# Kernel tuning notes

Hardware: AMD Instinct MI355X
Metric: run time of the kernel (lower is better)

Reference implementation:

```python
import jax, jax.numpy as jnp
import numpy as np

WIDTH = 32
DEPTH = 4
N_NODES = 50000
N_EDGES = 1600000


def setup_inputs() -> dict:
    key = jax.random.key(0)
    ks = jax.random.split(key, 10)
    N, E, W = N_NODES, N_EDGES, WIDTH
    s = 0.1
    x = jax.random.normal(ks[0], (N, 3), dtype=jnp.float32)
    edge_index = jax.random.randint(ks[1], (2, E), 0, N, dtype=jnp.int64)
    edge_attr = jax.random.uniform(ks[2], (E, 3), dtype=jnp.float32)
    # fc1: Linear(3, W); fc2: Linear(W, 1)
    fc1_w = jax.random.normal(ks[3], (W, 3), dtype=jnp.float32) * s
    fc1_b = jnp.zeros((W,), jnp.float32)
    fc2_w = jax.random.normal(ks[4], (1, W), dtype=jnp.float32) * s
    fc2_b = jnp.zeros((1,), jnp.float32)
    # 3 structurally distinct NNConv layers (reused DEPTH times), stacked on axis 0.
    # Edge-kernel MLP: Linear(3, W//4) -> ReLU -> Linear(W//4, W)
    kw1 = jax.random.normal(ks[5], (3, W // 4, 3), dtype=jnp.float32) * s
    kb1 = jnp.zeros((3, W // 4), jnp.float32)
    kw2 = jax.random.normal(ks[6], (3, W, W // 4), dtype=jnp.float32) * s
    kb2 = jnp.zeros((3, W), jnp.float32)
    # NNConv root weight [in, out] and bias
    root = jax.random.normal(ks[7], (3, W, W), dtype=jnp.float32) * s
    cbias = jnp.zeros((3, W), jnp.float32)
    return {"x": x, "edge_index": edge_index, "edge_attr": edge_attr,
            "fc1_w": fc1_w, "fc1_b": fc1_b, "fc2_w": fc2_w, "fc2_b": fc2_b,
            "kw1": kw1, "kb1": kb1, "kw2": kw2, "kb2": kb2,
            "root": root, "cbias": cbias}


def reference(x, edge_index, edge_attr, fc1_w, fc1_b, fc2_w, fc2_b,
              kw1, kb1, kw2, kb2, root, cbias):
    N = x.shape[0]
    src, dst = edge_index[0], edge_index[1]
    # in-degree counts for scatter-mean (clamped to 1 like PyG)
    counts = jax.ops.segment_sum(jnp.ones(dst.shape[0], x.dtype), dst, num_segments=N)
    inv_counts = 1.0 / jnp.maximum(counts, 1.0)

    h = x @ fc1_w.T + fc1_b  # [N, W]
    for _ in range(DEPTH):
        for c in range(3):
            # diagonal NNConv: edge MLP -> per-edge weight vector [E, W]
            w = jax.nn.relu(edge_attr @ kw1[c].T + kb1[c]) @ kw2[c].T + kb2[c]
            msg = h[src] * w                      # gather + elementwise per-edge product
            agg = jax.ops.segment_sum(msg, dst, num_segments=N) * inv_counts[:, None]
            h = jax.nn.relu(agg + h @ root[c] + cbias[c])
    return h @ fc2_w.T + fc2_b  # [N, 1]
```

## Files before the change

kernel.cpp:

```cpp
#include <hip/hip_runtime.h>

#define WN 32
#define HID 8
#define DEPTH 4
#define GPB 16

typedef float fvec4 __attribute__((ext_vector_type(4)));

__global__ void zero_kernel(int* __restrict__ cnt, int* __restrict__ cursor, int n) {
    int i = blockIdx.x * blockDim.x + threadIdx.x;
    if (i < n) { cnt[i] = 0; cursor[i] = 0; }
}

__global__ void count_kernel(const int* __restrict__ eidx, int* __restrict__ cnt, int e_cnt) {
    int e = blockIdx.x * blockDim.x + threadIdx.x;
    if (e >= e_cnt) return;
    atomicAdd(&cnt[eidx[e_cnt + e]], 1);
}

__global__ void scan_kernel(const int* __restrict__ cnt, int* __restrict__ row_ptr,
                            float* __restrict__ inv, int n) {
    __shared__ int s_wave[16];
    int t = threadIdx.x;
    int lane = t & 63;
    int wv = t >> 6;
    int offset = 0;
    for (int base = 0; base < n; base += 1024) {
        int i = base + t;
        int v = (i < n) ? cnt[i] : 0;
        int x = v;
#pragma unroll
        for (int d = 1; d < 64; d <<= 1) {
            int y = __shfl_up(x, d, 64);
            if (lane >= d) x += y;
        }
        if (lane == 63) s_wave[wv] = x;
        __syncthreads();
        if (wv == 0 && lane < 16) {
            int y = s_wave[lane];
#pragma unroll
            for (int d = 1; d < 16; d <<= 1) {
                int z = __shfl_up(y, d, 64);
                if (lane >= d) y += z;
            }
            s_wave[lane] = y;
        }
        __syncthreads();
        int waveoff = (wv > 0) ? s_wave[wv - 1] : 0;
        int total = s_wave[15];
        int incl = x + waveoff + offset;
        if (i < n) {
            row_ptr[i + 1] = incl;
            inv[i] = 1.0f / (float)(v > 1 ? v : 1);
        }
        offset += total;
        __syncthreads();
    }
    if (t == 0) row_ptr[0] = 0;
}

__global__ void scatter_kernel(const int* __restrict__ eidx, const float* __restrict__ ea,
                               const int* __restrict__ row_ptr, int* __restrict__ cursor,
                               fvec4* __restrict__ rec, int e_cnt) {
    int e = blockIdx.x * blockDim.x + threadIdx.x;
    if (e >= e_cnt) return;
    int src = eidx[e];
    int dst = eidx[e_cnt + e];
    int pos = row_ptr[dst] + atomicAdd(&cursor[dst], 1);
    fvec4 r;
    r.x = __int_as_float(src);
    r.y = ea[3 * e];
    r.z = ea[3 * e + 1];
    r.w = ea[3 * e + 2];
    rec[pos] = r;
}

__global__ void h0_kernel(const float* __restrict__ x, const float* __restrict__ fc1_w,
                          const float* __restrict__ fc1_b, float* __restrict__ h, int n) {
    __shared__ float s_w[WN * 3];
    __shared__ float s_b[WN];
    int t = threadIdx.x;
    if (t < WN * 3) s_w[t] = fc1_w[t];
    if (t < WN) s_b[t] = fc1_b[t];
    __syncthreads();
    int i = blockIdx.x * blockDim.x + t;
    if (i >= n) return;
    float x0 = x[3 * i], x1 = x[3 * i + 1], x2 = x[3 * i + 2];
#pragma unroll
    for (int j = 0; j < WN; j++) {
        h[(size_t)i * WN + j] = s_b[j] + s_w[j * 3] * x0 + s_w[j * 3 + 1] * x1 + s_w[j * 3 + 2] * x2;
    }
}

__global__ void gather2_kernel(const int* __restrict__ row_ptr, const fvec4* __restrict__ rec,
                               const float* __restrict__ h_in, float* __restrict__ h_out,
                               const float* __restrict__ inv,
                               const float* __restrict__ kw1, const float* __restrict__ kb1,
                               const float* __restrict__ kw2, const float* __restrict__ kb2,
                               const float* __restrict__ root, const float* __restrict__ cbias,
                               int n) {
    __shared__ float s_root[WN * 34];
    __shared__ float s_h[GPB * 34];
    __shared__ int   s_src[GPB][33];
    __shared__ fvec4 s_hid_u[GPB][33];
    __shared__ fvec4 s_hid_v[GPB][33];
    __shared__ int   s_maxdeg;

    int t = threadIdx.x;
    if (t == 0) s_maxdeg = 0;
    for (int i = t; i < WN * WN; i += 256) s_root[(i >> 5) * 34 + (i & 31)] = root[i];

    int grp = t >> 4;
    int tc  = t & 15;
    int node = blockIdx.x * GPB + grp;
    bool valid = node < n;

    const fvec4* kwp = (const fvec4*)(kw2 + tc * 16);
    fvec4 wa0 = kwp[0], wa1 = kwp[1];
    fvec4 wb0 = kwp[2], wb1 = kwp[3];
    float2 b2 = *(const float2*)(kb2 + 2 * tc);
    float2 cb = *(const float2*)(cbias + 2 * tc);

    int e0 = 0, e1 = 0;
    float2 hself = {0.0f, 0.0f};
    if (valid) {
        e0 = row_ptr[node];
        e1 = row_ptr[node + 1];
        hself = *(const float2*)(h_in + (size_t)node * WN + 2 * tc);
    }
    *(float2*)&s_h[grp * 34 + 2 * tc] = hself;
    int deg = e1 - e0;
    __syncthreads();
    if (valid && tc == 0 && deg > 0) atomicMax(&s_maxdeg, deg);
    __syncthreads();
    int nchunk = (s_maxdeg + 31) >> 5;

    float acc0 = 0.0f, acc1 = 0.0f;
    for (int cs = 0; cs < nchunk; cs++) {
        int ebase = e0 + (cs << 5);
#pragma unroll
        for (int s = 0; s < 2; s++) {
            int li = tc + (s << 4);
            int e = ebase + li;
            if (e < e1) {
                fvec4 r = rec[e];
                s_src[grp][li] = __float_as_int(r.x);
                float hv[HID];
#pragma unroll
                for (int j = 0; j < HID; j++) {
                    float u = kb1[j] + kw1[3 * j] * r.y + kw1[3 * j + 1] * r.z + kw1[3 * j + 2] * r.w;
                    hv[j] = u > 0.0f ? u : 0.0f;
                }
                fvec4 lo, hi;
                lo.x = hv[0]; lo.y = hv[1]; lo.z = hv[2]; lo.w = hv[3];
                hi.x = hv[4]; hi.y = hv[5]; hi.z = hv[6]; hi.w = hv[7];
                s_hid_u[grp][li] = lo;
                s_hid_v[grp][li] = hi;
            }
        }
        __syncthreads();
        int rem = e1 - ebase;
        int cnt = rem < 32 ? rem : 32;
#pragma unroll 4
        for (int i = 0; i < cnt; i++) {
            int src = s_src[grp][i];
            fvec4 u = s_hid_u[grp][i];
            fvec4 v = s_hid_v[grp][i];
            float w0 = b2.x + wa0.x * u.x + wa0.y * u.y + wa0.z * u.z + wa0.w * u.w
                            + wa1.x * v.x + wa1.y * v.y + wa1.z * v.z + wa1.w * v.w;
            float w1 = b2.y + wb0.x * u.x + wb0.y * u.y + wb0.z * u.z + wb0.w * u.w
                            + wb1.x * v.x + wb1.y * v.y + wb1.z * v.z + wb1.w * v.w;
            float2 hh = *(const float2*)(h_in + (size_t)src * WN + 2 * tc);
            acc0 += hh.x * w0;
            acc1 += hh.y * w1;
        }
        __syncthreads();
    }
    if (!valid) return;

    float invn = inv[node];
    float r0 = acc0 * invn + cb.x;
    float r1 = acc1 * invn + cb.y;
#pragma unroll
    for (int k = 0; k < WN; k++) {
        float hk = s_h[grp * 34 + k];
        float2 rt = *(const float2*)&s_root[k * 34 + 2 * tc];
        r0 += hk * rt.x;
        r1 += hk * rt.y;
    }
    float2 o;
    o.x = r0 > 0.0f ? r0 : 0.0f;
    o.y = r1 > 0.0f ? r1 : 0.0f;
    *(float2*)(h_out + (size_t)node * WN + 2 * tc) = o;
}

__global__ void out_kernel(const float* __restrict__ h, const float* __restrict__ fc2_w,
                           const float* __restrict__ fc2_b, float* __restrict__ out, int n) {
    __shared__ float s_w[WN];
    __shared__ float s_b;
    int t = threadIdx.x;
    if (t < WN) s_w[t] = fc2_w[t];
    if (t == 0) s_b = fc2_b[0];
    __syncthreads();
    int i = blockIdx.x * blockDim.x + t;
    if (i >= n) return;
    float acc = s_b;
#pragma unroll
    for (int k = 0; k < WN; k++) acc += h[(size_t)i * WN + k] * s_w[k];
    out[i] = acc;
}

extern "C" void kernel_launch(void* const* d_in, const int* in_sizes, int n_in,
                              void* d_out, int out_size, void* d_ws, size_t ws_size,
                              hipStream_t stream) {
    const float* x      = (const float*)d_in[0];
    const int*   eidx   = (const int*)d_in[1];
    const float* ea     = (const float*)d_in[2];
    const float* fc1_w  = (const float*)d_in[3];
    const float* fc1_b  = (const float*)d_in[4];
    const float* fc2_w  = (const float*)d_in[5];
    const float* fc2_b  = (const float*)d_in[6];
    const float* kw1    = (const float*)d_in[7];
    const float* kb1    = (const float*)d_in[8];
    const float* kw2    = (const float*)d_in[9];
    const float* kb2    = (const float*)d_in[10];
    const float* root   = (const float*)d_in[11];
    const float* cbias  = (const float*)d_in[12];
    float* out = (float*)d_out;

    const int n = in_sizes[0] / 3;
    const int e_cnt = in_sizes[2] / 3;

    auto pad4 = [](size_t v) { return (v + 3) & ~(size_t)3; };
    float* ws = (float*)d_ws;
    size_t off = 0;
    float* hA       = ws + off; off += pad4((size_t)n * WN);
    float* hB       = ws + off; off += pad4((size_t)n * WN);
    float* inv      = ws + off; off += pad4(n);
    int*   cnt      = (int*)(ws + off); off += pad4(n);
    int*   cursor   = (int*)(ws + off); off += pad4(n);
    int*   row_ptr  = (int*)(ws + off); off += pad4(n + 1);
    fvec4* rec      = (fvec4*)(ws + off); off += (size_t)4 * e_cnt;

    const int B = 256;
    int grid_n  = (n + B - 1) / B;
    int grid_e  = (e_cnt + B - 1) / B;
    int grid_g  = (n + GPB - 1) / GPB;

    zero_kernel<<<grid_n, B, 0, stream>>>(cnt, cursor, n);
    count_kernel<<<grid_e, B, 0, stream>>>(eidx, cnt, e_cnt);
    scan_kernel<<<1, 1024, 0, stream>>>(cnt, row_ptr, inv, n);
    scatter_kernel<<<grid_e, B, 0, stream>>>(eidx, ea, row_ptr, cursor, rec, e_cnt);
    h0_kernel<<<grid_n, B, 0, stream>>>(x, fc1_w, fc1_b, hA, n);

    float* hin = hA;
    float* hout = hB;
    for (int d = 0; d < DEPTH; d++) {
        for (int c = 0; c < 3; c++) {
            gather2_kernel<<<grid_g, B, 0, stream>>>(
                row_ptr, rec, hin, hout, inv,
                kw1 + (size_t)c * HID * 3, kb1 + (size_t)c * HID,
                kw2 + (size_t)c * WN * HID, kb2 + (size_t)c * WN,
                root + (size_t)c * WN * WN, cbias + (size_t)c * WN, n);
            float* tmp = hin; hin = hout; hout = tmp;
        }
    }
    out_kernel<<<grid_n, B, 0, stream>>>(hin, fc2_w, fc2_b, out, n);
}
```

Before: 764.0 us.

## Sort nodes by in-degree for load-balanced gather and drop shared root staging

Adds a degree histogram, a bin scan and an ordering pass so each gather block processes 16 nodes with similar in-degree, which cuts wasted iterations up to the block's max degree. It also drops the per-block shared-memory copy of the root matrix and reads root from global/L1 inside the final matvec. The cost is three extra preprocessing kernels, scattered node accesses through the order indirection, and possibly more global loads in the root product.

```diff
diff --git a/kernel.cpp b/kernel.cpp
--- a/kernel.cpp
+++ b/kernel.cpp
@@ -4,12 +4,15 @@
 #define HID 8
 #define DEPTH 4
 #define GPB 16
+#define NBIN 1024
 
 typedef float fvec4 __attribute__((ext_vector_type(4)));
 
-__global__ void zero_kernel(int* __restrict__ cnt, int* __restrict__ cursor, int n) {
+__global__ void zero_kernel(int* __restrict__ cnt, int* __restrict__ cursor,
+                            int* __restrict__ bins, int* __restrict__ bin_cursor, int n) {
     int i = blockIdx.x * blockDim.x + threadIdx.x;
     if (i < n) { cnt[i] = 0; cursor[i] = 0; }
+    if (i < NBIN) { bins[i] = 0; bin_cursor[i] = 0; }
 }
 
 __global__ void count_kernel(const int* __restrict__ eidx, int* __restrict__ cnt, int e_cnt) {
@@ -19,7 +22,7 @@
 }
 
 __global__ void scan_kernel(const int* __restrict__ cnt, int* __restrict__ row_ptr,
-                            float* __restrict__ inv, int n) {
+                            float* __restrict__ inv, int* __restrict__ bins, int n) {
     __shared__ int s_wave[16];
     int t = threadIdx.x;
     int lane = t & 63;
@@ -52,11 +55,51 @@
         if (i < n) {
             row_ptr[i + 1] = incl;
             inv[i] = 1.0f / (float)(v > 1 ? v : 1);
+            int d = v < (NBIN - 1) ? v : (NBIN - 1);
+            atomicAdd(&bins[d], 1);
         }
         offset += total;
         __syncthreads();
     }
     if (t == 0) row_ptr[0] = 0;
+}
+
+__global__ void bin_scan_kernel(const int* __restrict__ bins, int* __restrict__ bin_base) {
+    __shared__ int s_wave[16];
+    int t = threadIdx.x;
+    int lane = t & 63;
+    int wv = t >> 6;
+    int v = bins[t];
+    int x = v;
+#pragma unroll
+    for (int d = 1; d < 64; d <<= 1) {
+        int y = __shfl_up(x, d, 64);
+        if (lane >= d) x += y;
+    }
+    if (lane == 63) s_wave[wv] = x;
+    __syncthreads();
+    if (wv == 0 && lane < 16) {
+        int y = s_wave[lane];
+#pragma unroll
+        for (int d = 1; d < 16; d <<= 1) {
+            int z = __shfl_up(y, d, 64);
+            if (lane >= d) y += z;
+        }
+        s_wave[lane] = y;
+    }
+    __syncthreads();
+    int waveoff = (wv > 0) ? s_wave[wv - 1] : 0;
+    bin_base[t] = x + waveoff - v;
+}
+
+__global__ void order_kernel(const int* __restrict__ cnt, const int* __restrict__ bin_base,
+                             int* __restrict__ bin_cursor, int* __restrict__ order, int n) {
+    int i = blockIdx.x * blockDim.x + threadIdx.x;
+    if (i >= n) return;
+    int v = cnt[i];
+    int d = v < (NBIN - 1) ? v : (NBIN - 1);
+    int pos = bin_base[d] + atomicAdd(&bin_cursor[d], 1);
+    order[pos] = i;
 }
 
 __global__ void scatter_kernel(const int* __restrict__ eidx, const float* __restrict__ ea,
@@ -93,13 +136,13 @@
 }
 
 __global__ void gather2_kernel(const int* __restrict__ row_ptr, const fvec4* __restrict__ rec,
+                               const int* __restrict__ order,
                                const float* __restrict__ h_in, float* __restrict__ h_out,
                                const float* __restrict__ inv,
                                const float* __restrict__ kw1, const float* __restrict__ kb1,
                                const float* __restrict__ kw2, const float* __restrict__ kb2,
                                const float* __restrict__ root, const float* __restrict__ cbias,
                                int n) {
-    __shared__ float s_root[WN * 34];
     __shared__ float s_h[GPB * 34];
     __shared__ int   s_src[GPB][33];
     __shared__ fvec4 s_hid_u[GPB][33];
@@ -108,12 +151,12 @@
 
     int t = threadIdx.x;
     if (t == 0) s_maxdeg = 0;
-    for (int i = t; i < WN * WN; i += 256) s_root[(i >> 5) * 34 + (i & 31)] = root[i];
 
     int grp = t >> 4;
     int tc  = t & 15;
-    int node = blockIdx.x * GPB + grp;
-    bool valid = node < n;
+    int idx = blockIdx.x * GPB + grp;
+    bool valid = idx < n;
+    int node = valid ? order[idx] : 0;
 
     const fvec4* kwp = (const fvec4*)(kw2 + tc * 16);
     fvec4 wa0 = kwp[0], wa1 = kwp[1];
@@ -184,7 +227,7 @@
 #pragma unroll
     for (int k = 0; k < WN; k++) {
         float hk = s_h[grp * 34 + k];
-        float2 rt = *(const float2*)&s_root[k * 34 + 2 * tc];
+        float2 rt = *(const float2*)(root + k * WN + 2 * tc);
         r0 += hk * rt.x;
         r1 += hk * rt.y;
     }
@@ -234,22 +277,28 @@
     auto pad4 = [](size_t v) { return (v + 3) & ~(size_t)3; };
     float* ws = (float*)d_ws;
     size_t off = 0;
-    float* hA       = ws + off; off += pad4((size_t)n * WN);
-    float* hB       = ws + off; off += pad4((size_t)n * WN);
-    float* inv      = ws + off; off += pad4(n);
-    int*   cnt      = (int*)(ws + off); off += pad4(n);
-    int*   cursor   = (int*)(ws + off); off += pad4(n);
-    int*   row_ptr  = (int*)(ws + off); off += pad4(n + 1);
-    fvec4* rec      = (fvec4*)(ws + off); off += (size_t)4 * e_cnt;
+    float* hA        = ws + off; off += pad4((size_t)n * WN);
+    float* hB        = ws + off; off += pad4((size_t)n * WN);
+    float* inv       = ws + off; off += pad4(n);
+    int*   cnt       = (int*)(ws + off); off += pad4(n);
+    int*   cursor    = (int*)(ws + off); off += pad4(n);
+    int*   row_ptr   = (int*)(ws + off); off += pad4(n + 1);
+    int*   order     = (int*)(ws + off); off += pad4(n);
+    int*   bins      = (int*)(ws + off); off += NBIN;
+    int*   bin_base  = (int*)(ws + off); off += NBIN;
+    int*   bin_cur   = (int*)(ws + off); off += NBIN;
+    fvec4* rec       = (fvec4*)(ws + off); off += (size_t)4 * e_cnt;
 
     const int B = 256;
     int grid_n  = (n + B - 1) / B;
     int grid_e  = (e_cnt + B - 1) / B;
     int grid_g  = (n + GPB - 1) / GPB;
 
-    zero_kernel<<<grid_n, B, 0, stream>>>(cnt, cursor, n);
+    zero_kernel<<<grid_n, B, 0, stream>>>(cnt, cursor, bins, bin_cur, n);
     count_kernel<<<grid_e, B, 0, stream>>>(eidx, cnt, e_cnt);
-    scan_kernel<<<1, 1024, 0, stream>>>(cnt, row_ptr, inv, n);
+    scan_kernel<<<1, 1024, 0, stream>>>(cnt, row_ptr, inv, bins, n);
+    bin_scan_kernel<<<1, 1024, 0, stream>>>(bins, bin_base);
+    order_kernel<<<grid_n, B, 0, stream>>>(cnt, bin_base, bin_cur, order, n);
     scatter_kernel<<<grid_e, B, 0, stream>>>(eidx, ea, row_ptr, cursor, rec, e_cnt);
     h0_kernel<<<grid_n, B, 0, stream>>>(x, fc1_w, fc1_b, hA, n);
 
@@ -258,7 +307,7 @@
     for (int d = 0; d < DEPTH; d++) {
         for (int c = 0; c < 3; c++) {
             gather2_kernel<<<grid_g, B, 0, stream>>>(
-                row_ptr, rec, hin, hout, inv,
+                row_ptr, rec, order, hin, hout, inv,
                 kw1 + (size_t)c * HID * 3, kb1 + (size_t)c * HID,
                 kw2 + (size_t)c * WN * HID, kb2 + (size_t)c * WN,
                 root + (size_t)c * WN * WN, cbias + (size_t)c * WN, n);
```

New measurement: 1.080 ms. 1.41x slower.

## Split message passing into edge-balanced gather with atomics plus node update kernel

Applied to the files above, without the earlier changes.

Replaces the node-per-group gather kernel with an edge-balanced kernel in which each 16-lane group processes a fixed 128-edge slice of the CSR. It writes per-destination partial sums directly, or with atomics at slice boundaries, into an aggregation buffer. A separate update kernel applies the mean, root matmul, bias and ReLU, and re-zeroes the buffer. The single-block scan is also replaced with a three-kernel multi-block scan. This removes the load imbalance and block-wide max-degree padding of the old design, at the cost of an extra kernel launch per layer, extra agg traffic, and a binary search per group.

```diff
diff --git a/kernel.cpp b/kernel.cpp
--- a/kernel.cpp
+++ b/kernel.cpp
@@ -3,13 +3,15 @@
 #define WN 32
 #define HID 8
 #define DEPTH 4
-#define GPB 16
+#define TS 128
 
 typedef float fvec4 __attribute__((ext_vector_type(4)));
 
-__global__ void zero_kernel(int* __restrict__ cnt, int* __restrict__ cursor, int n) {
+__global__ void zero_kernel(int* __restrict__ cnt, int* __restrict__ cursor,
+                            float* __restrict__ agg, int n, int nagg) {
     int i = blockIdx.x * blockDim.x + threadIdx.x;
     if (i < n) { cnt[i] = 0; cursor[i] = 0; }
+    if (i < nagg) agg[i] = 0.0f;
 }
 
 __global__ void count_kernel(const int* __restrict__ eidx, int* __restrict__ cnt, int e_cnt) {
@@ -18,16 +20,27 @@
     atomicAdd(&cnt[eidx[e_cnt + e]], 1);
 }
 
-__global__ void scan_kernel(const int* __restrict__ cnt, int* __restrict__ row_ptr,
-                            float* __restrict__ inv, int n) {
-    __shared__ int s_wave[16];
-    int t = threadIdx.x;
-    int lane = t & 63;
-    int wv = t >> 6;
+__global__ void scan1_kernel(const int* __restrict__ cnt, int* __restrict__ blk_sum, int n) {
+    __shared__ int s_wave[4];
+    int t = threadIdx.x;
+    int lane = t & 63, wv = t >> 6;
+    int i = blockIdx.x * 256 + t;
+    int v = (i < n) ? cnt[i] : 0;
+#pragma unroll
+    for (int d = 1; d < 64; d <<= 1) v += __shfl_xor(v, d, 64);
+    if (lane == 0) s_wave[wv] = v;
+    __syncthreads();
+    if (t == 0) blk_sum[blockIdx.x] = s_wave[0] + s_wave[1] + s_wave[2] + s_wave[3];
+}
+
+__global__ void scan2_kernel(const int* __restrict__ blk_sum, int* __restrict__ blk_base, int nblk) {
+    __shared__ int s_wave[4];
+    int t = threadIdx.x;
+    int lane = t & 63, wv = t >> 6;
     int offset = 0;
-    for (int base = 0; base < n; base += 1024) {
+    for (int base = 0; base < nblk; base += 256) {
         int i = base + t;
-        int v = (i < n) ? cnt[i] : 0;
+        int v = (i < nblk) ? blk_sum[i] : 0;
         int x = v;
 #pragma unroll
         for (int d = 1; d < 64; d <<= 1) {
@@ -36,10 +49,10 @@
         }
         if (lane == 63) s_wave[wv] = x;
         __syncthreads();
-        if (wv == 0 && lane < 16) {
+        if (wv == 0 && lane < 4) {
             int y = s_wave[lane];
 #pragma unroll
-            for (int d = 1; d < 16; d <<= 1) {
+            for (int d = 1; d < 4; d <<= 1) {
                 int z = __shfl_up(y, d, 64);
                 if (lane >= d) y += z;
             }
@@ -47,16 +60,44 @@
         }
         __syncthreads();
         int waveoff = (wv > 0) ? s_wave[wv - 1] : 0;
-        int total = s_wave[15];
-        int incl = x + waveoff + offset;
-        if (i < n) {
-            row_ptr[i + 1] = incl;
-            inv[i] = 1.0f / (float)(v > 1 ? v : 1);
-        }
+        int total = s_wave[3];
+        if (i < nblk) blk_base[i] = x + waveoff + offset - v;
         offset += total;
         __syncthreads();
     }
-    if (t == 0) row_ptr[0] = 0;
+}
+
+__global__ void scan3_kernel(const int* __restrict__ cnt, const int* __restrict__ blk_base,
+                             int* __restrict__ row_ptr, float* __restrict__ inv, int n) {
+    __shared__ int s_wave[4];
+    int t = threadIdx.x;
+    int lane = t & 63, wv = t >> 6;
+    int i = blockIdx.x * 256 + t;
+    int v = (i < n) ? cnt[i] : 0;
+    int x = v;
+#pragma unroll
+    for (int d = 1; d < 64; d <<= 1) {
+        int y = __shfl_up(x, d, 64);
+        if (lane >= d) x += y;
+    }
+    if (lane == 63) s_wave[wv] = x;
+    __syncthreads();
+    if (wv == 0 && lane < 4) {
+        int y = s_wave[lane];
+#pragma unroll
+        for (int d = 1; d < 4; d <<= 1) {
+            int z = __shfl_up(y, d, 64);
+            if (lane >= d) y += z;
+        }
+        s_wave[lane] = y;
+    }
+    __syncthreads();
+    int waveoff = (wv > 0) ? s_wave[wv - 1] : 0;
+    if (i < n) {
+        row_ptr[i + 1] = blk_base[blockIdx.x] + waveoff + x;
+        inv[i] = 1.0f / (float)(v > 1 ? v : 1);
+    }
+    if (i == 0) row_ptr[0] = 0;
 }
 
 __global__ void scatter_kernel(const int* __restrict__ eidx, const float* __restrict__ ea,
@@ -92,80 +133,61 @@
     }
 }
 
-__global__ void gather2_kernel(const int* __restrict__ row_ptr, const fvec4* __restrict__ rec,
-                               const float* __restrict__ h_in, float* __restrict__ h_out,
-                               const float* __restrict__ inv,
-                               const float* __restrict__ kw1, const float* __restrict__ kb1,
-                               const float* __restrict__ kw2, const float* __restrict__ kb2,
-                               const float* __restrict__ root, const float* __restrict__ cbias,
-                               int n) {
-    __shared__ float s_root[WN * 34];
-    __shared__ float s_h[GPB * 34];
-    __shared__ int   s_src[GPB][33];
-    __shared__ fvec4 s_hid_u[GPB][33];
-    __shared__ fvec4 s_hid_v[GPB][33];
-    __shared__ int   s_maxdeg;
-
-    int t = threadIdx.x;
-    if (t == 0) s_maxdeg = 0;
-    for (int i = t; i < WN * WN; i += 256) s_root[(i >> 5) * 34 + (i & 31)] = root[i];
-
-    int grp = t >> 4;
-    int tc  = t & 15;
-    int node = blockIdx.x * GPB + grp;
-    bool valid = node < n;
+__global__ void gather_edge_kernel(const int* __restrict__ row_ptr, const fvec4* __restrict__ rec,
+                                   const float* __restrict__ h_in, float* __restrict__ agg,
+                                   const float* __restrict__ kw1, const float* __restrict__ kb1,
+                                   const float* __restrict__ kw2, const float* __restrict__ kb2,
+                                   int n, int e_cnt) {
+    __shared__ int   s_src[16][17];
+    __shared__ fvec4 s_u[16][17];
+    __shared__ fvec4 s_v[16][17];
+    int t = threadIdx.x;
+    int g = t >> 4, tc = t & 15;
+    long gid = (long)blockIdx.x * 16 + g;
+    int a = (int)(gid * TS);
+    if (a >= e_cnt) return;
+    int b = a + TS;
+    if (b > e_cnt) b = e_cnt;
 
     const fvec4* kwp = (const fvec4*)(kw2 + tc * 16);
     fvec4 wa0 = kwp[0], wa1 = kwp[1];
     fvec4 wb0 = kwp[2], wb1 = kwp[3];
     float2 b2 = *(const float2*)(kb2 + 2 * tc);
-    float2 cb = *(const float2*)(cbias + 2 * tc);
-
-    int e0 = 0, e1 = 0;
-    float2 hself = {0.0f, 0.0f};
-    if (valid) {
-        e0 = row_ptr[node];
-        e1 = row_ptr[node + 1];
-        hself = *(const float2*)(h_in + (size_t)node * WN + 2 * tc);
-    }
-    *(float2*)&s_h[grp * 34 + 2 * tc] = hself;
-    int deg = e1 - e0;
-    __syncthreads();
-    if (valid && tc == 0 && deg > 0) atomicMax(&s_maxdeg, deg);
-    __syncthreads();
-    int nchunk = (s_maxdeg + 31) >> 5;
+
+    int lo = 0, hi = n - 1;
+    while (lo < hi) {
+        int mid = (lo + hi + 1) >> 1;
+        if (row_ptr[mid] <= a) lo = mid; else hi = mid - 1;
+    }
+    int dst = lo;
+    int next_end = row_ptr[dst + 1];
+    bool seg_plain = (row_ptr[dst] == a);
 
     float acc0 = 0.0f, acc1 = 0.0f;
-    for (int cs = 0; cs < nchunk; cs++) {
-        int ebase = e0 + (cs << 5);
-#pragma unroll
-        for (int s = 0; s < 2; s++) {
-            int li = tc + (s << 4);
-            int e = ebase + li;
-            if (e < e1) {
-                fvec4 r = rec[e];
-                s_src[grp][li] = __float_as_int(r.x);
-                float hv[HID];
-#pragma unroll
-                for (int j = 0; j < HID; j++) {
-                    float u = kb1[j] + kw1[3 * j] * r.y + kw1[3 * j + 1] * r.z + kw1[3 * j + 2] * r.w;
-                    hv[j] = u > 0.0f ? u : 0.0f;
-                }
-                fvec4 lo, hi;
-                lo.x = hv[0]; lo.y = hv[1]; lo.z = hv[2]; lo.w = hv[3];
-                hi.x = hv[4]; hi.y = hv[5]; hi.z = hv[6]; hi.w = hv[7];
-                s_hid_u[grp][li] = lo;
-                s_hid_v[grp][li] = hi;
+    for (int sb = a; sb < b; sb += 16) {
+        int e = sb + tc;
+        if (e < b) {
+            fvec4 r = rec[e];
+            s_src[g][tc] = __float_as_int(r.x);
+            float hv[HID];
+#pragma unroll
+            for (int j = 0; j < HID; j++) {
+                float u = kb1[j] + kw1[3 * j] * r.y + kw1[3 * j + 1] * r.z + kw1[3 * j + 2] * r.w;
+                hv[j] = u > 0.0f ? u : 0.0f;
             }
-        }
-        __syncthreads();
-        int rem = e1 - ebase;
-        int cnt = rem < 32 ? rem : 32;
-#pragma unroll 4
-        for (int i = 0; i < cnt; i++) {
-            int src = s_src[grp][i];
-            fvec4 u = s_hid_u[grp][i];
-            fvec4 v = s_hid_v[grp][i];
+            fvec4 lo4, hi4;
+            lo4.x = hv[0]; lo4.y = hv[1]; lo4.z = hv[2]; lo4.w = hv[3];
+            hi4.x = hv[4]; hi4.y = hv[5]; hi4.z = hv[6]; hi4.w = hv[7];
+            s_u[g][tc] = lo4;
+            s_v[g][tc] = hi4;
+        }
+        __builtin_amdgcn_wave_barrier();
+        int cnt = b - sb;
+        if (cnt > 16) cnt = 16;
+        for (int j = 0; j < cnt; j++) {
+            int src = s_src[g][j];
+            fvec4 u = s_u[g][j];
+            fvec4 v = s_v[g][j];
             float w0 = b2.x + wa0.x * u.x + wa0.y * u.y + wa0.z * u.z + wa0.w * u.w
                             + wa1.x * v.x + wa1.y * v.y + wa1.z * v.z + wa1.w * v.w;
             float w1 = b2.y + wb0.x * u.x + wb0.y * u.y + wb0.z * u.z + wb0.w * u.w
@@ -173,25 +195,48 @@
             float2 hh = *(const float2*)(h_in + (size_t)src * WN + 2 * tc);
             acc0 += hh.x * w0;
             acc1 += hh.y * w1;
-        }
-        __syncthreads();
-    }
-    if (!valid) return;
-
-    float invn = inv[node];
-    float r0 = acc0 * invn + cb.x;
-    float r1 = acc1 * invn + cb.y;
-#pragma unroll
-    for (int k = 0; k < WN; k++) {
-        float hk = s_h[grp * 34 + k];
-        float2 rt = *(const float2*)&s_root[k * 34 + 2 * tc];
-        r0 += hk * rt.x;
-        r1 += hk * rt.y;
-    }
-    float2 o;
-    o.x = r0 > 0.0f ? r0 : 0.0f;
-    o.y = r1 > 0.0f ? r1 : 0.0f;
-    *(float2*)(h_out + (size_t)node * WN + 2 * tc) = o;
+            int enext = sb + j + 1;
+            if (enext == next_end) {
+                float* ap = agg + (size_t)dst * WN + 2 * tc;
+                if (seg_plain) { ap[0] = acc0; ap[1] = acc1; }
+                else { atomicAdd(ap, acc0); atomicAdd(ap + 1, acc1); }
+                acc0 = 0.0f; acc1 = 0.0f;
+                seg_plain = true;
+                dst++;
+                while (dst < n && row_ptr[dst + 1] == enext) dst++;
+                next_end = (dst < n) ? row_ptr[dst + 1] : 0x7FFFFFFF;
+            }
+        }
+        __builtin_amdgcn_wave_barrier();
+    }
+    if (b < next_end) {
+        float* ap = agg + (size_t)dst * WN + 2 * tc;
+        atomicAdd(ap, acc0);
+        atomicAdd(ap + 1, acc1);
+    }
+}
+
+__global__ void update_kernel(const float* __restrict__ h_in, float* __restrict__ h_out,
+                              float* __restrict__ agg, const float* __restrict__ inv,
+                              const float* __restrict__ root, const float* __restrict__ cbias,
+                              int n) {
+    __shared__ float s_root[WN * WN];
+    __shared__ float s_h[8][WN];
+    int t = threadIdx.x;
+    for (int i = t; i < WN * WN; i += 256) s_root[i] = root[i];
+    int grp = t >> 5, ch = t & 31;
+    int node = blockIdx.x * 8 + grp;
+    float hval = (node < n) ? h_in[(size_t)node * WN + ch] : 0.0f;
+    s_h[grp][ch] = hval;
+    __syncthreads();
+    if (node >= n) return;
+    size_t idx = (size_t)node * WN + ch;
+    float acc = agg[idx] * inv[node] + cbias[ch];
+    agg[idx] = 0.0f;
+    const float* srow = s_h[grp];
+#pragma unroll
+    for (int k = 0; k < WN; k++) acc += srow[k] * s_root[k * WN + ch];
+    h_out[idx] = acc > 0.0f ? acc : 0.0f;
 }
 
 __global__ void out_kernel(const float* __restrict__ h, const float* __restrict__ fc2_w,
@@ -236,20 +281,30 @@
     size_t off = 0;
     float* hA       = ws + off; off += pad4((size_t)n * WN);
     float* hB       = ws + off; off += pad4((size_t)n * WN);
+    float* agg      = ws + off; off += pad4((size_t)n * WN);
     float* inv      = ws + off; off += pad4(n);
     int*   cnt      = (int*)(ws + off); off += pad4(n);
     int*   cursor   = (int*)(ws + off); off += pad4(n);
     int*   row_ptr  = (int*)(ws + off); off += pad4(n + 1);
+    int*   blk_sum  = (int*)(ws + off); off += pad4((n + 255) / 256);
+    int*   blk_base = (int*)(ws + off); off += pad4((n + 255) / 256);
     fvec4* rec      = (fvec4*)(ws + off); off += (size_t)4 * e_cnt;
 
     const int B = 256;
+    int nagg    = n * WN;
+    int grid_nw = (nagg + B - 1) / B;
     int grid_n  = (n + B - 1) / B;
     int grid_e  = (e_cnt + B - 1) / B;
-    int grid_g  = (n + GPB - 1) / GPB;
-
-    zero_kernel<<<grid_n, B, 0, stream>>>(cnt, cursor, n);
+    int nblk    = (n + 255) / 256;
+    int ngroups = (e_cnt + TS - 1) / TS;
+    int grid_ge = (ngroups + 15) / 16;
+    int grid_u  = (n + 7) / 8;
+
+    zero_kernel<<<grid_nw, B, 0, stream>>>(cnt, cursor, agg, n, nagg);
     count_kernel<<<grid_e, B, 0, stream>>>(eidx, cnt, e_cnt);
-    scan_kernel<<<1, 1024, 0, stream>>>(cnt, row_ptr, inv, n);
+    scan1_kernel<<<nblk, B, 0, stream>>>(cnt, blk_sum, n);
+    scan2_kernel<<<1, B, 0, stream>>>(blk_sum, blk_base, nblk);
+    scan3_kernel<<<nblk, B, 0, stream>>>(cnt, blk_base, row_ptr, inv, n);
     scatter_kernel<<<grid_e, B, 0, stream>>>(eidx, ea, row_ptr, cursor, rec, e_cnt);
     h0_kernel<<<grid_n, B, 0, stream>>>(x, fc1_w, fc1_b, hA, n);
 
@@ -257,10 +312,12 @@
     float* hout = hB;
     for (int d = 0; d < DEPTH; d++) {
         for (int c = 0; c < 3; c++) {
-            gather2_kernel<<<grid_g, B, 0, stream>>>(
-                row_ptr, rec, hin, hout, inv,
+            gather_edge_kernel<<<grid_ge, B, 0, stream>>>(
+                row_ptr, rec, hin, agg,
                 kw1 + (size_t)c * HID * 3, kb1 + (size_t)c * HID,
-                kw2 + (size_t)c * WN * HID, kb2 + (size_t)c * WN,
+                kw2 + (size_t)c * WN * HID, kb2 + (size_t)c * WN, n, e_cnt);
+            update_kernel<<<grid_u, B, 0, stream>>>(
+                hin, hout, agg, inv,
                 root + (size_t)c * WN * WN, cbias + (size_t)c * WN, n);
             float* tmp = hin; hin = hout; hout = tmp;
         }
```

Result: slower. 1.186 ms (+55.2%).

## Parallelize degree scan across blocks and widen gather to 4 channels per thread

Applied to the files above, without the earlier changes.

Replaces the single-block serial prefix scan over node degrees with a three-pass multi-block scan (block sums, scan of sums, local scan plus offset). The gather kernel now processes 32 nodes per block with 8 threads per node, each handling 4 output channels via float4 loads. Edges are staged in chunks of 16, which halves the thread count per node and doubles per-thread edge-weight MLP arithmetic and register use. The aim is to cut the serial scan latency and make the neighbor feature gathers wider while amortizing edge-hidden computation over more channels.

```diff
diff --git a/kernel.cpp b/kernel.cpp
--- a/kernel.cpp
+++ b/kernel.cpp
@@ -3,7 +3,7 @@
 #define WN 32
 #define HID 8
 #define DEPTH 4
-#define GPB 16
+#define GPB 32
 
 typedef float fvec4 __attribute__((ext_vector_type(4)));
 
@@ -18,16 +18,27 @@
     atomicAdd(&cnt[eidx[e_cnt + e]], 1);
 }
 
-__global__ void scan_kernel(const int* __restrict__ cnt, int* __restrict__ row_ptr,
-                            float* __restrict__ inv, int n) {
-    __shared__ int s_wave[16];
-    int t = threadIdx.x;
-    int lane = t & 63;
-    int wv = t >> 6;
+__global__ void scan1_kernel(const int* __restrict__ cnt, int* __restrict__ blk_sum, int n) {
+    __shared__ int s_wave[4];
+    int t = threadIdx.x;
+    int lane = t & 63, wv = t >> 6;
+    int i = blockIdx.x * 256 + t;
+    int v = (i < n) ? cnt[i] : 0;
+#pragma unroll
+    for (int d = 1; d < 64; d <<= 1) v += __shfl_xor(v, d, 64);
+    if (lane == 0) s_wave[wv] = v;
+    __syncthreads();
+    if (t == 0) blk_sum[blockIdx.x] = s_wave[0] + s_wave[1] + s_wave[2] + s_wave[3];
+}
+
+__global__ void scan2_kernel(const int* __restrict__ blk_sum, int* __restrict__ blk_base, int nblk) {
+    __shared__ int s_wave[4];
+    int t = threadIdx.x;
+    int lane = t & 63, wv = t >> 6;
     int offset = 0;
-    for (int base = 0; base < n; base += 1024) {
+    for (int base = 0; base < nblk; base += 256) {
         int i = base + t;
-        int v = (i < n) ? cnt[i] : 0;
+        int v = (i < nblk) ? blk_sum[i] : 0;
         int x = v;
 #pragma unroll
         for (int d = 1; d < 64; d <<= 1) {
@@ -36,10 +47,10 @@
         }
         if (lane == 63) s_wave[wv] = x;
         __syncthreads();
-        if (wv == 0 && lane < 16) {
+        if (wv == 0 && lane < 4) {
             int y = s_wave[lane];
 #pragma unroll
-            for (int d = 1; d < 16; d <<= 1) {
+            for (int d = 1; d < 4; d <<= 1) {
                 int z = __shfl_up(y, d, 64);
                 if (lane >= d) y += z;
             }
@@ -47,16 +58,44 @@
         }
         __syncthreads();
         int waveoff = (wv > 0) ? s_wave[wv - 1] : 0;
-        int total = s_wave[15];
-        int incl = x + waveoff + offset;
-        if (i < n) {
-            row_ptr[i + 1] = incl;
-            inv[i] = 1.0f / (float)(v > 1 ? v : 1);
-        }
+        int total = s_wave[3];
+        if (i < nblk) blk_base[i] = x + waveoff + offset - v;
         offset += total;
         __syncthreads();
     }
-    if (t == 0) row_ptr[0] = 0;
+}
+
+__global__ void scan3_kernel(const int* __restrict__ cnt, const int* __restrict__ blk_base,
+                             int* __restrict__ row_ptr, float* __restrict__ inv, int n) {
+    __shared__ int s_wave[4];
+    int t = threadIdx.x;
+    int lane = t & 63, wv = t >> 6;
+    int i = blockIdx.x * 256 + t;
+    int v = (i < n) ? cnt[i] : 0;
+    int x = v;
+#pragma unroll
+    for (int d = 1; d < 64; d <<= 1) {
+        int y = __shfl_up(x, d, 64);
+        if (lane >= d) x += y;
+    }
+    if (lane == 63) s_wave[wv] = x;
+    __syncthreads();
+    if (wv == 0 && lane < 4) {
+        int y = s_wave[lane];
+#pragma unroll
+        for (int d = 1; d < 4; d <<= 1) {
+            int z = __shfl_up(y, d, 64);
+            if (lane >= d) y += z;
+        }
+        s_wave[lane] = y;
+    }
+    __syncthreads();
+    int waveoff = (wv > 0) ? s_wave[wv - 1] : 0;
+    if (i < n) {
+        row_ptr[i + 1] = blk_base[blockIdx.x] + waveoff + x;
+        inv[i] = 1.0f / (float)(v > 1 ? v : 1);
+    }
+    if (i == 0) row_ptr[0] = 0;
 }
 
 __global__ void scatter_kernel(const int* __restrict__ eidx, const float* __restrict__ ea,
@@ -92,55 +131,57 @@
     }
 }
 
-__global__ void gather2_kernel(const int* __restrict__ row_ptr, const fvec4* __restrict__ rec,
+__global__ void gather4_kernel(const int* __restrict__ row_ptr, const fvec4* __restrict__ rec,
                                const float* __restrict__ h_in, float* __restrict__ h_out,
                                const float* __restrict__ inv,
                                const float* __restrict__ kw1, const float* __restrict__ kb1,
                                const float* __restrict__ kw2, const float* __restrict__ kb2,
                                const float* __restrict__ root, const float* __restrict__ cbias,
                                int n) {
-    __shared__ float s_root[WN * 34];
-    __shared__ float s_h[GPB * 34];
-    __shared__ int   s_src[GPB][33];
-    __shared__ fvec4 s_hid_u[GPB][33];
-    __shared__ fvec4 s_hid_v[GPB][33];
+    __shared__ float s_root[WN * 36];
+    __shared__ float s_h[GPB * 36];
+    __shared__ int   s_src[GPB][17];
+    __shared__ fvec4 s_u[GPB][17];
+    __shared__ fvec4 s_v[GPB][17];
     __shared__ int   s_maxdeg;
 
     int t = threadIdx.x;
     if (t == 0) s_maxdeg = 0;
-    for (int i = t; i < WN * WN; i += 256) s_root[(i >> 5) * 34 + (i & 31)] = root[i];
-
-    int grp = t >> 4;
-    int tc  = t & 15;
+    for (int i = t; i < WN * WN; i += 256) s_root[(i >> 5) * 36 + (i & 31)] = root[i];
+
+    int grp = t >> 3;
+    int tc  = t & 7;
     int node = blockIdx.x * GPB + grp;
     bool valid = node < n;
 
-    const fvec4* kwp = (const fvec4*)(kw2 + tc * 16);
-    fvec4 wa0 = kwp[0], wa1 = kwp[1];
-    fvec4 wb0 = kwp[2], wb1 = kwp[3];
-    float2 b2 = *(const float2*)(kb2 + 2 * tc);
-    float2 cb = *(const float2*)(cbias + 2 * tc);
+    const fvec4* kwp = (const fvec4*)(kw2 + tc * 32);
+    fvec4 w0a = kwp[0], w0b = kwp[1];
+    fvec4 w1a = kwp[2], w1b = kwp[3];
+    fvec4 w2a = kwp[4], w2b = kwp[5];
+    fvec4 w3a = kwp[6], w3b = kwp[7];
+    fvec4 b2 = *(const fvec4*)(kb2 + 4 * tc);
+    fvec4 cb = *(const fvec4*)(cbias + 4 * tc);
 
     int e0 = 0, e1 = 0;
-    float2 hself = {0.0f, 0.0f};
+    fvec4 hself = {0.0f, 0.0f, 0.0f, 0.0f};
     if (valid) {
         e0 = row_ptr[node];
         e1 = row_ptr[node + 1];
-        hself = *(const float2*)(h_in + (size_t)node * WN + 2 * tc);
-    }
-    *(float2*)&s_h[grp * 34 + 2 * tc] = hself;
+        hself = *(const fvec4*)(h_in + (size_t)node * WN + 4 * tc);
+    }
+    *(fvec4*)&s_h[grp * 36 + 4 * tc] = hself;
     int deg = e1 - e0;
     __syncthreads();
     if (valid && tc == 0 && deg > 0) atomicMax(&s_maxdeg, deg);
     __syncthreads();
-    int nchunk = (s_maxdeg + 31) >> 5;
-
-    float acc0 = 0.0f, acc1 = 0.0f;
+    int nchunk = (s_maxdeg + 15) >> 4;
+
+    fvec4 acc = {0.0f, 0.0f, 0.0f, 0.0f};
     for (int cs = 0; cs < nchunk; cs++) {
-        int ebase = e0 + (cs << 5);
+        int ebase = e0 + (cs << 4);
 #pragma unroll
         for (int s = 0; s < 2; s++) {
-            int li = tc + (s << 4);
+            int li = tc + (s << 3);
             int e = ebase + li;
             if (e < e1) {
                 fvec4 r = rec[e];
@@ -151,47 +192,60 @@
                     float u = kb1[j] + kw1[3 * j] * r.y + kw1[3 * j + 1] * r.z + kw1[3 * j + 2] * r.w;
                     hv[j] = u > 0.0f ? u : 0.0f;
                 }
-                fvec4 lo, hi;
-                lo.x = hv[0]; lo.y = hv[1]; lo.z = hv[2]; lo.w = hv[3];
-                hi.x = hv[4]; hi.y = hv[5]; hi.z = hv[6]; hi.w = hv[7];
-                s_hid_u[grp][li] = lo;
-                s_hid_v[grp][li] = hi;
+                fvec4 lo4, hi4;
+                lo4.x = hv[0]; lo4.y = hv[1]; lo4.z = hv[2]; lo4.w = hv[3];
+                hi4.x = hv[4]; hi4.y = hv[5]; hi4.z = hv[6]; hi4.w = hv[7];
+                s_u[grp][li] = lo4;
+                s_v[grp][li] = hi4;
             }
         }
         __syncthreads();
         int rem = e1 - ebase;
-        int cnt = rem < 32 ? rem : 32;
+        int cnt = rem < 16 ? rem : 16;
 #pragma unroll 4
         for (int i = 0; i < cnt; i++) {
             int src = s_src[grp][i];
-            fvec4 u = s_hid_u[grp][i];
-            fvec4 v = s_hid_v[grp][i];
-            float w0 = b2.x + wa0.x * u.x + wa0.y * u.y + wa0.z * u.z + wa0.w * u.w
-                            + wa1.x * v.x + wa1.y * v.y + wa1.z * v.z + wa1.w * v.w;
-            float w1 = b2.y + wb0.x * u.x + wb0.y * u.y + wb0.z * u.z + wb0.w * u.w
-                            + wb1.x * v.x + wb1.y * v.y + wb1.z * v.z + wb1.w * v.w;
-            float2 hh = *(const float2*)(h_in + (size_t)src * WN + 2 * tc);
-            acc0 += hh.x * w0;
-            acc1 += hh.y * w1;
+            fvec4 u = s_u[grp][i];
+            fvec4 v = s_v[grp][i];
+            float w0 = b2.x + w0a.x * u.x + w0a.y * u.y + w0a.z * u.z + w0a.w * u.w
+                            + w0b.x * v.x + w0b.y * v.y + w0b.z * v.z + w0b.w * v.w;
+            float w1 = b2.y + w1a.x * u.x + w1a.y * u.y + w1a.z * u.z + w1a.w * u.w
+                            + w1b.x * v.x + w1b.y * v.y + w1b.z * v.z + w1b.w * v.w;
+            float w2 = b2.z + w2a.x * u.x + w2a.y * u.y + w2a.z * u.z + w2a.w * u.w
+                            + w2b.x * v.x + w2b.y * v.y + w2b.z * v.z + w2b.w * v.w;
+            float w3 = b2.w + w3a.x * u.x + w3a.y * u.y + w3a.z * u.z + w3a.w * u.w
+                            + w3b.x * v.x + w3b.y * v.y + w3b.z * v.z + w3b.w * v.w;
+            fvec4 hh = *(const fvec4*)(h_in + (size_t)src * WN + 4 * tc);
+            acc.x += hh.x * w0;
+            acc.y += hh.y * w1;
+            acc.z += hh.z * w2;
+            acc.w += hh.w * w3;
         }
         __syncthreads();
     }
     if (!valid) return;
 
     float invn = inv[node];
-    float r0 = acc0 * invn + cb.x;
-    float r1 = acc1 * invn + cb.y;
+    fvec4 r;
+    r.x = acc.x * invn + cb.x;
+    r.y = acc.y * invn + cb.y;
+    r.z = acc.z * invn + cb.z;
+    r.w = acc.w * invn + cb.w;
 #pragma unroll
     for (int k = 0; k < WN; k++) {
-        float hk = s_h[grp * 34 + k];
-        float2 rt = *(const float2*)&s_root[k * 34 + 2 * tc];
-        r0 += hk * rt.x;
-        r1 += hk * rt.y;
-    }
-    float2 o;
-    o.x = r0 > 0.0f ? r0 : 0.0f;
-    o.y = r1 > 0.0f ? r1 : 0.0f;
-    *(float2*)(h_out + (size_t)node * WN + 2 * tc) = o;
+        float hk = s_h[grp * 36 + k];
+        fvec4 rt = *(const fvec4*)&s_root[k * 36 + 4 * tc];
+        r.x += hk * rt.x;
+        r.y += hk * rt.y;
+        r.z += hk * rt.z;
+        r.w += hk * rt.w;
+    }
+    fvec4 o;
+    o.x = r.x > 0.0f ? r.x : 0.0f;
+    o.y = r.y > 0.0f ? r.y : 0.0f;
+    o.z = r.z > 0.0f ? r.z : 0.0f;
+    o.w = r.w > 0.0f ? r.w : 0.0f;
+    *(fvec4*)(h_out + (size_t)node * WN + 4 * tc) = o;
 }
 
 __global__ void out_kernel(const float* __restrict__ h, const float* __restrict__ fc2_w,
@@ -240,16 +294,21 @@
     int*   cnt      = (int*)(ws + off); off += pad4(n);
     int*   cursor   = (int*)(ws + off); off += pad4(n);
     int*   row_ptr  = (int*)(ws + off); off += pad4(n + 1);
+    int*   blk_sum  = (int*)(ws + off); off += pad4((n + 255) / 256);
+    int*   blk_base = (int*)(ws + off); off += pad4((n + 255) / 256);
     fvec4* rec      = (fvec4*)(ws + off); off += (size_t)4 * e_cnt;
 
     const int B = 256;
     int grid_n  = (n + B - 1) / B;
     int grid_e  = (e_cnt + B - 1) / B;
+    int nblk    = (n + 255) / 256;
     int grid_g  = (n + GPB - 1) / GPB;
 
     zero_kernel<<<grid_n, B, 0, stream>>>(cnt, cursor, n);
     count_kernel<<<grid_e, B, 0, stream>>>(eidx, cnt, e_cnt);
-    scan_kernel<<<1, 1024, 0, stream>>>(cnt, row_ptr, inv, n);
+    scan1_kernel<<<nblk, B, 0, stream>>>(cnt, blk_sum, n);
+    scan2_kernel<<<1, B, 0, stream>>>(blk_sum, blk_base, nblk);
+    scan3_kernel<<<nblk, B, 0, stream>>>(cnt, blk_base, row_ptr, inv, n);
     scatter_kernel<<<grid_e, B, 0, stream>>>(eidx, ea, row_ptr, cursor, rec, e_cnt);
     h0_kernel<<<grid_n, B, 0, stream>>>(x, fc1_w, fc1_b, hA, n);
 
@@ -257,7 +316,7 @@
     float* hout = hB;
     for (int d = 0; d < DEPTH; d++) {
         for (int c = 0; c < 3; c++) {
-            gather2_kernel<<<grid_g, B, 0, stream>>>(
+            gather4_kernel<<<grid_g, B, 0, stream>>>(
                 row_ptr, rec, hin, hout, inv,
                 kw1 + (size_t)c * HID * 3, kb1 + (size_t)c * HID,
                 kw2 + (size_t)c * WN * HID, kb2 + (size_t)c * WN,
```

Result: slower. 822.9 us (+7.7%).
